# Kernel tuning notes

Hardware: AMD Instinct MI355X
Metric: run time of the kernel (lower is better)

The kernel has to match this reference:

```python
import jax, jax.numpy as jnp
import numpy as np

DT = 0.01
NJ = 7
GRAV = 9.81
Q_LOWER = jnp.array([-2.9671, -1.8326, -2.9671, -3.1416, -2.9671, -0.0873, -2.9671], jnp.float32)
Q_UPPER = jnp.array([ 2.9671,  1.8326,  2.9671,  0.0,     2.9671,  3.8223,  2.9671], jnp.float32)


def _skew(v):
    z = jnp.zeros((), v.dtype)
    return jnp.stack([jnp.stack([z, -v[2], v[1]]),
                      jnp.stack([v[2], z, -v[0]]),
                      jnp.stack([-v[1], v[0], z])])


def _mot_X(E, r):
    # 6x6 spatial motion transform [[E,0],[-E*skew(r),E]]
    zero = jnp.zeros_like(E)
    top = jnp.concatenate([E, zero], axis=1)
    bot = jnp.concatenate([-E @ _skew(r), E], axis=1)
    return jnp.concatenate([top, bot], axis=0)


def _crm(v):
    # spatial motion cross-product matrix for v=[w;v0]
    Sw, Sv = _skew(v[:3]), _skew(v[3:])
    zero = jnp.zeros_like(Sw)
    top = jnp.concatenate([Sw, zero], axis=1)
    bot = jnp.concatenate([Sv, Sw], axis=1)
    return jnp.concatenate([top, bot], axis=0)


def _step_single(x, u, axes, R_tree, p_tree, I_sp):
    dt_ = x.dtype
    q = jnp.clip(x[:NJ], Q_LOWER.astype(dt_), Q_UPPER.astype(dt_))
    qd = x[NJ:]
    # forward kinematics: per-joint 6x6 child<-parent transforms and motion subspaces
    Xups, Ss = [], []
    eye3 = jnp.eye(3, dtype=dt_)
    for i in range(NJ):
        a = axes[i]
        c, s = jnp.cos(q[i]), jnp.sin(q[i])
        R = c * eye3 + s * _skew(a) + (1.0 - c) * jnp.outer(a, a)  # rodrigues
        Xj = _mot_X(R.T, jnp.zeros(3, dt_))
        Xt = _mot_X(R_tree[i], p_tree[i])
        Xups.append(Xj @ Xt)
        Ss.append(jnp.concatenate([a, jnp.zeros(3, dt_)]))
    # RNEA bias force h (qdd=0, gravity, zero base velocity, identity base pose)
    v_prev = jnp.zeros(6, dt_)
    a_prev = jnp.array([0.0, 0.0, 0.0, 0.0, 0.0, GRAV], dt_)  # a_base = -g trick
    fs = []
    for i in range(NJ):
        vJ = Ss[i] * qd[i]
        v = Xups[i] @ v_prev + vJ
        acc = Xups[i] @ a_prev + _crm(v) @ vJ
        Iv = I_sp[i] @ v
        f = I_sp[i] @ acc - _crm(v).T @ Iv  # crf(v) = -crm(v)^T
        fs.append(f)
        v_prev, a_prev = v, acc
    h = [None] * NJ
    for i in range(NJ - 1, -1, -1):
        h[i] = Ss[i] @ fs[i]
        if i > 0:
            fs[i - 1] = fs[i - 1] + Xups[i].T @ fs[i]
    h = jnp.stack(h)
    # CRBA mass matrix (serial chain, parent(i)=i-1)
    Ic = [I_sp[i] for i in range(NJ)]
    M = jnp.zeros((NJ, NJ), dt_)
    for i in range(NJ - 1, -1, -1):
        if i > 0:
            Ic[i - 1] = Ic[i - 1] + Xups[i].T @ Ic[i] @ Xups[i]
        F = Ic[i] @ Ss[i]
        M = M.at[i, i].set(Ss[i] @ F)
        for j in range(i - 1, -1, -1):
            F = Xups[j + 1].T @ F
            mij = Ss[j] @ F
            M = M.at[i, j].set(mij).at[j, i].set(mij)
    M = M + 1e-8 * jnp.eye(NJ, dtype=dt_)
    qdd = jnp.linalg.solve(M, (u - h)[:, None])[:, 0]
    qd_new = qd + DT * qdd
    q_new = q + DT * qd_new
    return jnp.concatenate([q_new, qd_new])


def setup_inputs() -> dict:
    B = 65536
    key = jax.random.key(0)
    k1, k2 = jax.random.split(key)
    x = jax.random.normal(k1, (B, 14), jnp.float32)
    u = jax.random.normal(k2, (B, 7), jnp.float32)
    rng = np.random.default_rng(0)
    # unit joint axes
    axes = rng.normal(size=(NJ, 3))
    axes = axes / np.linalg.norm(axes, axis=1, keepdims=True)
    # orthonormal fixed parent->child rotations (det +1)
    R_tree = np.empty((NJ, 3, 3))
    for i in range(NJ):
        Q, _ = np.linalg.qr(rng.normal(size=(3, 3)))
        if np.linalg.det(Q) < 0:
            Q[:, 0] = -Q[:, 0]
        R_tree[i] = Q
    p_tree = 0.2 * rng.normal(size=(NJ, 3))
    # SPD 6x6 spatial inertias: [[Ibar, m*Cx],[m*Cx^T, m*I3]]
    I_sp = np.empty((NJ, 6, 6))
    for i in range(NJ):
        m = float(rng.uniform(1.0, 5.0))
        c = 0.05 * rng.normal(size=3)
        Cx = np.array([[0, -c[2], c[1]], [c[2], 0, -c[0]], [-c[1], c[0], 0]])
        A = 0.1 * rng.normal(size=(3, 3))
        Ic_ = A @ A.T + 0.05 * np.eye(3)
        Ibar = Ic_ + m * Cx @ Cx.T
        I_sp[i] = np.block([[Ibar, m * Cx], [m * Cx.T, m * np.eye(3)]])
    return {
        "x": x, "u": u,
        "axes": jnp.asarray(axes, jnp.float32),
        "R_tree": jnp.asarray(R_tree, jnp.float32),
        "p_tree": jnp.asarray(p_tree, jnp.float32),
        "I_sp": jnp.asarray(I_sp, jnp.float32),
    }


def reference(x, u, axes, R_tree, p_tree, I_sp):
    return jax.vmap(_step_single, in_axes=(0, 0, None, None, None, None))(
        x, u, axes, R_tree, p_tree, I_sp)
```

## Files before the change

kernel.cpp:

```cpp
#include <hip/hip_runtime.h>
#include <math.h>

#define NJ 7
#define DTF 0.01f
#define GRAVF 9.81f
#define MIX(i,j) ((i)*((i)+1)/2 + (j))
#define SNC  15
#define QST  9

__device__ __forceinline__ void cross3(const float* a, const float* b, float* o){
    o[0] = a[1]*b[2] - a[2]*b[1];
    o[1] = a[2]*b[0] - a[0]*b[2];
    o[2] = a[0]*b[1] - a[1]*b[0];
}
__device__ __forceinline__ void mv3(const float* E, const float* x, float* y){
    y[0] = E[0]*x[0] + E[1]*x[1] + E[2]*x[2];
    y[1] = E[3]*x[0] + E[4]*x[1] + E[5]*x[2];
    y[2] = E[6]*x[0] + E[7]*x[1] + E[8]*x[2];
}
__device__ __forceinline__ void mtv3(const float* E, const float* x, float* y){
    y[0] = E[0]*x[0] + E[3]*x[1] + E[6]*x[2];
    y[1] = E[1]*x[0] + E[4]*x[1] + E[7]*x[2];
    y[2] = E[2]*x[0] + E[5]*x[1] + E[8]*x[2];
}
__device__ __forceinline__ void symv(const float* S, const float* x, float* y){
    y[0] = S[0]*x[0] + S[1]*x[1] + S[2]*x[2];
    y[1] = S[1]*x[0] + S[3]*x[1] + S[4]*x[2];
    y[2] = S[2]*x[0] + S[4]*x[1] + S[5]*x[2];
}
__device__ __forceinline__ void mm3(const float* A, const float* B, float* o){
#pragma unroll
    for (int r = 0; r < 3; r++)
#pragma unroll
        for (int c = 0; c < 3; c++)
            o[r*3+c] = A[r*3]*B[c] + A[r*3+1]*B[3+c] + A[r*3+2]*B[6+c];
}
__device__ __forceinline__ void congr(const float* E, const float* X, float* o){
    float t[9];
#pragma unroll
    for (int r = 0; r < 3; r++)
#pragma unroll
        for (int c = 0; c < 3; c++)
            t[r*3+c] = E[r]*X[c] + E[3+r]*X[3+c] + E[6+r]*X[6+c];
    mm3(t, E, o);
}
__device__ __forceinline__ void makeE(const float* a, const float* __restrict__ Rt,
                                      float s, float c, float* E){
    float omc = 1.0f - c;
    float RT[9];
    RT[0] = c + omc*a[0]*a[0];       RT[1] =  s*a[2] + omc*a[0]*a[1]; RT[2] = -s*a[1] + omc*a[0]*a[2];
    RT[3] = -s*a[2] + omc*a[1]*a[0]; RT[4] = c + omc*a[1]*a[1];       RT[5] =  s*a[0] + omc*a[1]*a[2];
    RT[6] =  s*a[1] + omc*a[2]*a[0]; RT[7] = -s*a[0] + omc*a[2]*a[1]; RT[8] = c + omc*a[2]*a[2];
    float Rl[9];
#pragma unroll
    for (int k = 0; k < 9; k++) Rl[k] = Rt[k];
    mm3(RT, Rl, E);
}
__device__ __forceinline__ void bodyI(const float* __restrict__ g_I, int i,
                                      float* SA, float* h, float& m){
    const float* I6 = g_I + i*36;
    SA[0]=I6[0]; SA[1]=I6[1]; SA[2]=I6[2];
    SA[3]=I6[7]; SA[4]=I6[8]; SA[5]=I6[14];
    h[0]=I6[16]; h[1]=I6[5]; h[2]=I6[9];
    m = I6[21];
}

__constant__ float QL_c[NJ] = {-2.9671f,-1.8326f,-2.9671f,-3.1416f,-2.9671f,-0.0873f,-2.9671f};
__constant__ float QU_c[NJ] = { 2.9671f, 1.8326f, 2.9671f, 0.0f,    2.9671f, 3.8223f, 2.9671f};

__global__ __launch_bounds__(128, 2)
void panda_step(const float* __restrict__ x, const float* __restrict__ u,
                const float* __restrict__ g_ax, const float* __restrict__ g_Rt,
                const float* __restrict__ g_pt, const float* __restrict__ g_I,
                float* __restrict__ out, int B)
{
    __shared__ float s_snc[64*SNC];
    __shared__ float s_q  [64*QST];
    __shared__ float s_qd [64*QST];
    __shared__ float s_rhs[64*QST];

    const int role = threadIdx.x >> 6;
    const int lane = threadIdx.x & 63;
    const int e    = blockIdx.x*64 + lane;
    const bool act = (e < B);

    float a_all[3*NJ], p_all[3*NJ];
#pragma unroll
    for (int j = 0; j < 3*NJ; j++){ a_all[j] = g_ax[j]; p_all[j] = g_pt[j]; }
    float SA[6], hc[3], mc;
    bodyI(g_I, 6, SA, hc, mc);

    float q[NJ], qd[NJ], sn[NJ], cs[NJ], uu[NJ];
    if (act && role == 0){
        const float2* x2 = (const float2*)(x + e*14);
        float xl[14];
#pragma unroll
        for (int i = 0; i < 7; i++){ float2 v = x2[i]; xl[2*i] = v.x; xl[2*i+1] = v.y; }
#pragma unroll
        for (int i = 0; i < NJ; i++){
            q[i]  = fminf(fmaxf(xl[i], QL_c[i]), QU_c[i]);
            qd[i] = xl[NJ + i];
            uu[i] = u[e*NJ + i];
            __sincosf(q[i], &sn[i], &cs[i]);
            s_snc[lane*SNC + i]     = sn[i];
            s_snc[lane*SNC + 7 + i] = cs[i];
            s_q [lane*QST + i]      = q[i];
            s_qd[lane*QST + i]      = qd[i];
        }
    }
    __syncthreads();

    float Mx[28];
    if (act){
      if (role == 1){
        float sn1[NJ], cs1[NJ];
#pragma unroll
        for (int i = 0; i < NJ; i++){
            sn1[i] = s_snc[lane*SNC + i];
            cs1[i] = s_snc[lane*SNC + 7 + i];
        }
        float Fb[6*NJ];
#pragma unroll
        for (int i = NJ-1; i >= 0; --i){
            float a[3] = { a_all[3*i], a_all[3*i+1], a_all[3*i+2] };
            float Ft[3]; symv(SA, a, Ft);
            Fb[i*6+0]=Ft[0]; Fb[i*6+1]=Ft[1]; Fb[i*6+2]=Ft[2];
            Fb[i*6+3] = a[1]*hc[2] - a[2]*hc[1];
            Fb[i*6+4] = a[2]*hc[0] - a[0]*hc[2];
            Fb[i*6+5] = a[0]*hc[1] - a[1]*hc[0];
#pragma unroll
            for (int k = i; k < NJ; ++k)
                Mx[MIX(k,i)] = a[0]*Fb[k*6] + a[1]*Fb[k*6+1] + a[2]*Fb[k*6+2];
            if (i > 0){
                float p[3] = { p_all[3*i], p_all[3*i+1], p_all[3*i+2] };
                float E[9]; makeE(a, g_Rt + 9*i, sn1[i], cs1[i], E);
                float SAm[6], hm[3], mm_;
                bodyI(g_I, i-1, SAm, hm, mm_);
                float Af[9] = {SA[0],SA[1],SA[2], SA[1],SA[3],SA[4], SA[2],SA[4],SA[5]};
                float Ap[9]; congr(E, Af, Ap);
                float hr[3]; mtv3(E, hc, hr);
                float hpd = hr[0]*p[0]+hr[1]*p[1]+hr[2]*p[2];
                float ppd = p[0]*p[0]+p[1]*p[1]+p[2]*p[2];
                float dga = 2.0f*hpd + mc*ppd;
                SA[0] = Ap[0] - 2.0f*p[0]*hr[0] - mc*p[0]*p[0] + dga + SAm[0];
                SA[1] = Ap[1] - p[0]*hr[1] - hr[0]*p[1] - mc*p[0]*p[1] + SAm[1];
                SA[2] = Ap[2] - p[0]*hr[2] - hr[0]*p[2] - mc*p[0]*p[2] + SAm[2];
                SA[3] = Ap[4] - 2.0f*p[1]*hr[1] - mc*p[1]*p[1] + dga + SAm[3];
                SA[4] = Ap[5] - p[1]*hr[2] - hr[1]*p[2] - mc*p[1]*p[2] + SAm[4];
                SA[5] = Ap[8] - 2.0f*p[2]*hr[2] - mc*p[2]*p[2] + dga + SAm[5];
                hc[0] = hr[0] + mc*p[0] + hm[0];
                hc[1] = hr[1] + mc*p[1] + hm[1];
                hc[2] = hr[2] + mc*p[2] + hm[2];
                mc += mm_;
#pragma unroll
                for (int k = i; k < NJ; ++k){
                    float ft[3] = {Fb[k*6+0], Fb[k*6+1], Fb[k*6+2]};
                    float fb2[3] = {Fb[k*6+3], Fb[k*6+4], Fb[k*6+5]};
                    float tm[3], tf[3], cp[3];
                    mtv3(E, ft, tm); mtv3(E, fb2, tf);
                    cross3(p, tf, cp);
                    Fb[k*6+0]=tm[0]+cp[0]; Fb[k*6+1]=tm[1]+cp[1]; Fb[k*6+2]=tm[2]+cp[2];
                    Fb[k*6+3]=tf[0];       Fb[k*6+4]=tf[1];       Fb[k*6+5]=tf[2];
                }
            }
        }
#pragma unroll
        for (int i = 0; i < NJ; i++) Mx[MIX(i,i)] += 1e-8f;
#pragma unroll
        for (int k = 0; k < NJ; k++){
            float d = Mx[MIX(k,k)];
#pragma unroll
            for (int j = 0; j < NJ; j++) if (j < k) d -= Mx[MIX(k,j)]*Mx[MIX(k,j)];
            float linv = __builtin_amdgcn_rsqf(d);
            Mx[MIX(k,k)] = linv;
#pragma unroll
            for (int i2 = k+1; i2 < NJ; i2++){
                float s2 = Mx[MIX(i2,k)];
#pragma unroll
                for (int j = 0; j < NJ; j++) if (j < k) s2 -= Mx[MIX(i2,j)]*Mx[MIX(k,j)];
                Mx[MIX(i2,k)] = s2 * linv;
            }
        }
      } else {
        float Fb[6*NJ];
        float w[3]  = {0.f,0.f,0.f}, vl[3] = {0.f,0.f,0.f};
        float aw[3] = {0.f,0.f,0.f}, avv[3] = {0.f,0.f,GRAVF};
#pragma unroll
        for (int i = 0; i < NJ; ++i){
            float a[3] = { a_all[3*i], a_all[3*i+1], a_all[3*i+2] };
            float p[3] = { p_all[3*i], p_all[3*i+1], p_all[3*i+2] };
            float qdi = qd[i];
            float E[9]; makeE(a, g_Rt + 9*i, sn[i], cs[i], E);
            float tw[3]; mv3(E, w, tw);
            float nw[3] = { tw[0]+a[0]*qdi, tw[1]+a[1]*qdi, tw[2]+a[2]*qdi };
            float cwp[3]; cross3(w, p, cwp);
            float t1[3] = { vl[0]+cwp[0], vl[1]+cwp[1], vl[2]+cwp[2] };
            float nvl[3]; mv3(E, t1, nvl);
            float taw[3]; mv3(E, aw, taw);
            float cna[3]; cross3(nw, a, cna);
            float naw[3] = { taw[0]+qdi*cna[0], taw[1]+qdi*cna[1], taw[2]+qdi*cna[2] };
            float cap[3]; cross3(aw, p, cap);
            float t2[3] = { avv[0]+cap[0], avv[1]+cap[1], avv[2]+cap[2] };
            float tav[3]; mv3(E, t2, tav);
            float cva[3]; cross3(nvl, a, cva);
            float nav[3] = { tav[0]+qdi*cva[0], tav[1]+qdi*cva[1], tav[2]+qdi*cva[2] };
            float SAi[6], hi[3], mi; bodyI(g_I, i, SAi, hi, mi);
            float Ivt[3], Iat[3], hxv[3], hxa[3];
            symv(SAi, nw, Ivt);  cross3(hi, nvl, hxv);
            symv(SAi, naw, Iat); cross3(hi, nav, hxa);
#pragma unroll
            for (int k = 0; k < 3; k++){ Ivt[k] += hxv[k]; Iat[k] += hxa[k]; }
            float hxw[3], hxaw[3];
            cross3(hi, nw, hxw); cross3(hi, naw, hxaw);
            float Ivb[3] = { mi*nvl[0]-hxw[0], mi*nvl[1]-hxw[1], mi*nvl[2]-hxw[2] };
            float Iab[3] = { mi*nav[0]-hxaw[0], mi*nav[1]-hxaw[1], mi*nav[2]-hxaw[2] };
            float c1[3], c2[3], c3[3];
            cross3(nw, Ivt, c1); cross3(nvl, Ivb, c2); cross3(nw, Ivb, c3);
            Fb[i*6+0] = Iat[0]+c1[0]+c2[0];
            Fb[i*6+1] = Iat[1]+c1[1]+c2[1];
            Fb[i*6+2] = Iat[2]+c1[2]+c2[2];
            Fb[i*6+3] = Iab[0]+c3[0];
            Fb[i*6+4] = Iab[1]+c3[1];
            Fb[i*6+5] = Iab[2]+c3[2];
#pragma unroll
            for (int k = 0; k < 3; k++){ w[k]=nw[k]; vl[k]=nvl[k]; aw[k]=naw[k]; avv[k]=nav[k]; }
        }
#pragma unroll
        for (int i = NJ-1; i >= 0; --i){
            float a[3] = { a_all[3*i], a_all[3*i+1], a_all[3*i+2] };
            float f0=Fb[i*6+0], f1=Fb[i*6+1], f2=Fb[i*6+2];
            s_rhs[lane*QST + i] = uu[i] - (a[0]*f0 + a[1]*f1 + a[2]*f2);
            if (i > 0){
                float p[3] = { p_all[3*i], p_all[3*i+1], p_all[3*i+2] };
                float E[9]; makeE(a, g_Rt + 9*i, sn[i], cs[i], E);
                float ftop[3] = {f0, f1, f2};
                float fbot[3] = {Fb[i*6+3], Fb[i*6+4], Fb[i*6+5]};
                float tm[3], tf[3], cp[3];
                mtv3(E, ftop, tm); mtv3(E, fbot, tf);
                cross3(p, tf, cp);
                Fb[(i-1)*6+0] += tm[0]+cp[0];
                Fb[(i-1)*6+1] += tm[1]+cp[1];
                Fb[(i-1)*6+2] += tm[2]+cp[2];
                Fb[(i-1)*6+3] += tf[0];
                Fb[(i-1)*6+4] += tf[1];
                Fb[(i-1)*6+5] += tf[2];
            }
        }
      }
    }

    __syncthreads();

    if (act && role == 1){
        float rhs[NJ];
#pragma unroll
        for (int i = 0; i < NJ; i++) rhs[i] = s_rhs[lane*QST + i];
        float y[NJ];
#pragma unroll
        for (int i = 0; i < NJ; i++){
            float s2 = rhs[i];
#pragma unroll
            for (int j = 0; j < NJ; j++) if (j < i) s2 -= Mx[MIX(i,j)]*y[j];
            y[i] = s2 * Mx[MIX(i,i)];
        }
        float z[NJ];
#pragma unroll
        for (int i = NJ-1; i >= 0; i--){
            float s2 = y[i];
#pragma unroll
            for (int j = NJ-1; j >= 0; j--) if (j > i) s2 -= Mx[MIX(j,i)]*z[j];
            z[i] = s2 * Mx[MIX(i,i)];
        }
        float o14[14];
#pragma unroll
        for (int i = 0; i < NJ; i++){
            float qv  = s_q [lane*QST + i];
            float qdv = s_qd[lane*QST + i];
            float qdn = qdv + DTF*z[i];
            o14[i]      = qv + DTF*qdn;
            o14[NJ + i] = qdn;
        }
        float2* o2 = (float2*)(out + e*14);
#pragma unroll
        for (int i = 0; i < 7; i++){ float2 v; v.x = o14[2*i]; v.y = o14[2*i+1]; o2[i] = v; }
    }
}

extern "C" void kernel_launch(void* const* d_in, const int* in_sizes, int n_in,
                              void* d_out, int out_size, void* d_ws, size_t ws_size,
                              hipStream_t stream) {
    const float* x   = (const float*)d_in[0];
    const float* u   = (const float*)d_in[1];
    const float* ax  = (const float*)d_in[2];
    const float* Rt  = (const float*)d_in[3];
    const float* pt  = (const float*)d_in[4];
    const float* Isp = (const float*)d_in[5];
    float* out = (float*)d_out;
    int B = in_sizes[0] / 14;
    int grid = (B + 63) / 64;
    hipLaunchKernelGGL(panda_step, dim3(grid), dim3(128), 0, stream,
                       x, u, ax, Rt, pt, Isp, out, B);
}
```

Before: 83.13 us.

## Roll joint loops and move per-joint state to LDS to cut registers

Replaces the fully unrolled joint loops with rolled loops that prefetch the next joint's axis, offset, rotation and inertia from global memory into registers one step ahead. The per-element force arrays and mass-matrix entries move from registers into padded shared-memory arrays, and the torque vector is staged in shared memory and updated in place. The aim is to lower VGPR pressure and spilling so more waves fit per CU. The cost is extra LDS traffic, loop overhead and less instruction-level parallelism from the loss of full unrolling.

```diff
diff --git a/kernel.cpp b/kernel.cpp
--- a/kernel.cpp
+++ b/kernel.cpp
@@ -5,8 +5,10 @@
 #define DTF 0.01f
 #define GRAVF 9.81f
 #define MIX(i,j) ((i)*((i)+1)/2 + (j))
+#define MPAD 29
+#define FSTR 43
 #define SNC  15
-#define QST  9
+#define MST  23
 
 __device__ __forceinline__ void cross3(const float* a, const float* b, float* o){
     o[0] = a[1]*b[2] - a[2]*b[1];
@@ -44,16 +46,13 @@
             t[r*3+c] = E[r]*X[c] + E[3+r]*X[3+c] + E[6+r]*X[6+c];
     mm3(t, E, o);
 }
-__device__ __forceinline__ void makeE(const float* a, const float* __restrict__ Rt,
-                                      float s, float c, float* E){
+__device__ __forceinline__ void makeE_reg(const float* a, const float* Rl,
+                                          float s, float c, float* E){
     float omc = 1.0f - c;
     float RT[9];
     RT[0] = c + omc*a[0]*a[0];       RT[1] =  s*a[2] + omc*a[0]*a[1]; RT[2] = -s*a[1] + omc*a[0]*a[2];
     RT[3] = -s*a[2] + omc*a[1]*a[0]; RT[4] = c + omc*a[1]*a[1];       RT[5] =  s*a[0] + omc*a[1]*a[2];
     RT[6] =  s*a[1] + omc*a[2]*a[0]; RT[7] = -s*a[0] + omc*a[2]*a[1]; RT[8] = c + omc*a[2]*a[2];
-    float Rl[9];
-#pragma unroll
-    for (int k = 0; k < 9; k++) Rl[k] = Rt[k];
     mm3(RT, Rl, E);
 }
 __device__ __forceinline__ void bodyI(const float* __restrict__ g_I, int i,
@@ -74,38 +73,51 @@
                 const float* __restrict__ g_pt, const float* __restrict__ g_I,
                 float* __restrict__ out, int B)
 {
-    __shared__ float s_snc[64*SNC];
-    __shared__ float s_q  [64*QST];
-    __shared__ float s_qd [64*QST];
-    __shared__ float s_rhs[64*QST];
+    __shared__ float s_M   [64*MPAD];
+    __shared__ float s_F   [2*64*FSTR];
+    __shared__ float s_snc [64*SNC];
+    __shared__ float s_misc[64*MST];
 
     const int role = threadIdx.x >> 6;
     const int lane = threadIdx.x & 63;
     const int e    = blockIdx.x*64 + lane;
     const bool act = (e < B);
 
-    float a_all[3*NJ], p_all[3*NJ];
-#pragma unroll
-    for (int j = 0; j < 3*NJ; j++){ a_all[j] = g_ax[j]; p_all[j] = g_pt[j]; }
+    float aC[3], pC[3], RC[9];
+    float SAx[6], hx[3], mx;
     float SA[6], hc[3], mc;
-    bodyI(g_I, 6, SA, hc, mc);
-
-    float q[NJ], qd[NJ], sn[NJ], cs[NJ], uu[NJ];
-    if (act && role == 0){
-        const float2* x2 = (const float2*)(x + e*14);
-        float xl[14];
-#pragma unroll
-        for (int i = 0; i < 7; i++){ float2 v = x2[i]; xl[2*i] = v.x; xl[2*i+1] = v.y; }
-#pragma unroll
-        for (int i = 0; i < NJ; i++){
-            q[i]  = fminf(fmaxf(xl[i], QL_c[i]), QU_c[i]);
-            qd[i] = xl[NJ + i];
-            uu[i] = u[e*NJ + i];
-            __sincosf(q[i], &sn[i], &cs[i]);
-            s_snc[lane*SNC + i]     = sn[i];
-            s_snc[lane*SNC + 7 + i] = cs[i];
-            s_q [lane*QST + i]      = q[i];
-            s_qd[lane*QST + i]      = qd[i];
+    float snC = 0.f, csC = 0.f, qdC = 0.f;
+
+    if (role == 1){
+        bodyI(g_I, 6, SA, hc, mc);
+        bodyI(g_I, 5, SAx, hx, mx);
+        aC[0]=g_ax[18]; aC[1]=g_ax[19]; aC[2]=g_ax[20];
+        pC[0]=g_pt[18]; pC[1]=g_pt[19]; pC[2]=g_pt[20];
+#pragma unroll
+        for (int k = 0; k < 9; k++) RC[k] = g_Rt[54+k];
+    } else {
+        bodyI(g_I, 0, SAx, hx, mx);
+        aC[0]=g_ax[0]; aC[1]=g_ax[1]; aC[2]=g_ax[2];
+        pC[0]=g_pt[0]; pC[1]=g_pt[1]; pC[2]=g_pt[2];
+#pragma unroll
+        for (int k = 0; k < 9; k++) RC[k] = g_Rt[k];
+        if (act){
+            const float2* x2 = (const float2*)(x + e*14);
+            float xl[14];
+#pragma unroll
+            for (int i = 0; i < 7; i++){ float2 v = x2[i]; xl[2*i] = v.x; xl[2*i+1] = v.y; }
+#pragma unroll
+            for (int i = 0; i < NJ; i++){
+                float qi  = fminf(fmaxf(xl[i], QL_c[i]), QU_c[i]);
+                float qdi = xl[NJ + i];
+                float s, c; __sincosf(qi, &s, &c);
+                s_snc [lane*SNC + i]      = s;
+                s_snc [lane*SNC + 7 + i]  = c;
+                s_misc[lane*MST + i]      = qi;
+                s_misc[lane*MST + 7 + i]  = qdi;
+                s_misc[lane*MST + 14 + i] = u[e*NJ + i];
+                if (i == 0){ snC = s; csC = c; qdC = qdi; }
+            }
         }
     }
     __syncthreads();
@@ -113,57 +125,71 @@
     float Mx[28];
     if (act){
       if (role == 1){
-        float sn1[NJ], cs1[NJ];
-#pragma unroll
-        for (int i = 0; i < NJ; i++){
-            sn1[i] = s_snc[lane*SNC + i];
-            cs1[i] = s_snc[lane*SNC + 7 + i];
-        }
-        float Fb[6*NJ];
-#pragma unroll
+        float* Fb = &s_F[64*FSTR + lane*FSTR];
+        snC = s_snc[lane*SNC + 6];
+        csC = s_snc[lane*SNC + 13];
+#pragma unroll 1
         for (int i = NJ-1; i >= 0; --i){
-            float a[3] = { a_all[3*i], a_all[3*i+1], a_all[3*i+2] };
-            float Ft[3]; symv(SA, a, Ft);
+            float aN[3], pN[3], RN[9], snN, csN, SAxN[6], hxN[3], mxN;
+            if (i > 0){
+                const int b3 = 3*(i-1), b9 = 9*(i-1);
+                aN[0]=g_ax[b3]; aN[1]=g_ax[b3+1]; aN[2]=g_ax[b3+2];
+                pN[0]=g_pt[b3]; pN[1]=g_pt[b3+1]; pN[2]=g_pt[b3+2];
+#pragma unroll
+                for (int k = 0; k < 9; k++) RN[k] = g_Rt[b9+k];
+                snN = s_snc[lane*SNC + (i-1)];
+                csN = s_snc[lane*SNC + 6 + i];
+                bodyI(g_I, (i >= 2) ? (i-2) : 0, SAxN, hxN, mxN);
+            }
+            float Ft[3]; symv(SA, aC, Ft);
             Fb[i*6+0]=Ft[0]; Fb[i*6+1]=Ft[1]; Fb[i*6+2]=Ft[2];
-            Fb[i*6+3] = a[1]*hc[2] - a[2]*hc[1];
-            Fb[i*6+4] = a[2]*hc[0] - a[0]*hc[2];
-            Fb[i*6+5] = a[0]*hc[1] - a[1]*hc[0];
-#pragma unroll
-            for (int k = i; k < NJ; ++k)
-                Mx[MIX(k,i)] = a[0]*Fb[k*6] + a[1]*Fb[k*6+1] + a[2]*Fb[k*6+2];
+            Fb[i*6+3] = aC[1]*hc[2] - aC[2]*hc[1];
+            Fb[i*6+4] = aC[2]*hc[0] - aC[0]*hc[2];
+            Fb[i*6+5] = aC[0]*hc[1] - aC[1]*hc[0];
+#pragma unroll 1
+            for (int k = i; k < NJ; ++k){
+                float f0=Fb[k*6], f1=Fb[k*6+1], f2=Fb[k*6+2];
+                s_M[lane*MPAD + k*(k+1)/2 + i] = aC[0]*f0 + aC[1]*f1 + aC[2]*f2;
+            }
             if (i > 0){
-                float p[3] = { p_all[3*i], p_all[3*i+1], p_all[3*i+2] };
-                float E[9]; makeE(a, g_Rt + 9*i, sn1[i], cs1[i], E);
-                float SAm[6], hm[3], mm_;
-                bodyI(g_I, i-1, SAm, hm, mm_);
+                float E[9]; makeE_reg(aC, RC, snC, csC, E);
                 float Af[9] = {SA[0],SA[1],SA[2], SA[1],SA[3],SA[4], SA[2],SA[4],SA[5]};
                 float Ap[9]; congr(E, Af, Ap);
                 float hr[3]; mtv3(E, hc, hr);
-                float hpd = hr[0]*p[0]+hr[1]*p[1]+hr[2]*p[2];
-                float ppd = p[0]*p[0]+p[1]*p[1]+p[2]*p[2];
+                float hpd = hr[0]*pC[0]+hr[1]*pC[1]+hr[2]*pC[2];
+                float ppd = pC[0]*pC[0]+pC[1]*pC[1]+pC[2]*pC[2];
                 float dga = 2.0f*hpd + mc*ppd;
-                SA[0] = Ap[0] - 2.0f*p[0]*hr[0] - mc*p[0]*p[0] + dga + SAm[0];
-                SA[1] = Ap[1] - p[0]*hr[1] - hr[0]*p[1] - mc*p[0]*p[1] + SAm[1];
-                SA[2] = Ap[2] - p[0]*hr[2] - hr[0]*p[2] - mc*p[0]*p[2] + SAm[2];
-                SA[3] = Ap[4] - 2.0f*p[1]*hr[1] - mc*p[1]*p[1] + dga + SAm[3];
-                SA[4] = Ap[5] - p[1]*hr[2] - hr[1]*p[2] - mc*p[1]*p[2] + SAm[4];
-                SA[5] = Ap[8] - 2.0f*p[2]*hr[2] - mc*p[2]*p[2] + dga + SAm[5];
-                hc[0] = hr[0] + mc*p[0] + hm[0];
-                hc[1] = hr[1] + mc*p[1] + hm[1];
-                hc[2] = hr[2] + mc*p[2] + hm[2];
-                mc += mm_;
-#pragma unroll
+                SA[0] = Ap[0] - 2.0f*pC[0]*hr[0] - mc*pC[0]*pC[0] + dga + SAx[0];
+                SA[1] = Ap[1] - pC[0]*hr[1] - hr[0]*pC[1] - mc*pC[0]*pC[1] + SAx[1];
+                SA[2] = Ap[2] - pC[0]*hr[2] - hr[0]*pC[2] - mc*pC[0]*pC[2] + SAx[2];
+                SA[3] = Ap[4] - 2.0f*pC[1]*hr[1] - mc*pC[1]*pC[1] + dga + SAx[3];
+                SA[4] = Ap[5] - pC[1]*hr[2] - hr[1]*pC[2] - mc*pC[1]*pC[2] + SAx[4];
+                SA[5] = Ap[8] - 2.0f*pC[2]*hr[2] - mc*pC[2]*pC[2] + dga + SAx[5];
+                hc[0] = hr[0] + mc*pC[0] + hx[0];
+                hc[1] = hr[1] + mc*pC[1] + hx[1];
+                hc[2] = hr[2] + mc*pC[2] + hx[2];
+                mc += mx;
+#pragma unroll 1
                 for (int k = i; k < NJ; ++k){
-                    float ft[3] = {Fb[k*6+0], Fb[k*6+1], Fb[k*6+2]};
+                    float ft[3]  = {Fb[k*6+0], Fb[k*6+1], Fb[k*6+2]};
                     float fb2[3] = {Fb[k*6+3], Fb[k*6+4], Fb[k*6+5]};
                     float tm[3], tf[3], cp[3];
                     mtv3(E, ft, tm); mtv3(E, fb2, tf);
-                    cross3(p, tf, cp);
+                    cross3(pC, tf, cp);
                     Fb[k*6+0]=tm[0]+cp[0]; Fb[k*6+1]=tm[1]+cp[1]; Fb[k*6+2]=tm[2]+cp[2];
                     Fb[k*6+3]=tf[0];       Fb[k*6+4]=tf[1];       Fb[k*6+5]=tf[2];
                 }
-            }
-        }
+#pragma unroll
+                for (int k = 0; k < 3; k++){ aC[k]=aN[k]; pC[k]=pN[k]; hx[k]=hxN[k]; }
+#pragma unroll
+                for (int k = 0; k < 9; k++) RC[k]=RN[k];
+#pragma unroll
+                for (int k = 0; k < 6; k++) SAx[k]=SAxN[k];
+                snC=snN; csC=csN; mx=mxN;
+            }
+        }
+#pragma unroll
+        for (int j = 0; j < 28; j++) Mx[j] = s_M[lane*MPAD + j];
 #pragma unroll
         for (int i = 0; i < NJ; i++) Mx[MIX(i,i)] += 1e-8f;
 #pragma unroll
@@ -182,38 +208,46 @@
             }
         }
       } else {
-        float Fb[6*NJ];
+        float* Fb = &s_F[lane*FSTR];
         float w[3]  = {0.f,0.f,0.f}, vl[3] = {0.f,0.f,0.f};
         float aw[3] = {0.f,0.f,0.f}, avv[3] = {0.f,0.f,GRAVF};
-#pragma unroll
+#pragma unroll 1
         for (int i = 0; i < NJ; ++i){
-            float a[3] = { a_all[3*i], a_all[3*i+1], a_all[3*i+2] };
-            float p[3] = { p_all[3*i], p_all[3*i+1], p_all[3*i+2] };
-            float qdi = qd[i];
-            float E[9]; makeE(a, g_Rt + 9*i, sn[i], cs[i], E);
+            float aN[3], pN[3], RN[9], snN, csN, qdN, SAxN[6], hxN[3], mxN;
+            if (i < NJ-1){
+                const int b3 = 3*(i+1), b9 = 9*(i+1);
+                aN[0]=g_ax[b3]; aN[1]=g_ax[b3+1]; aN[2]=g_ax[b3+2];
+                pN[0]=g_pt[b3]; pN[1]=g_pt[b3+1]; pN[2]=g_pt[b3+2];
+#pragma unroll
+                for (int k = 0; k < 9; k++) RN[k] = g_Rt[b9+k];
+                snN = s_snc [lane*SNC + i + 1];
+                csN = s_snc [lane*SNC + 8 + i];
+                qdN = s_misc[lane*MST + 8 + i];
+                bodyI(g_I, i+1, SAxN, hxN, mxN);
+            }
+            float E[9]; makeE_reg(aC, RC, snC, csC, E);
             float tw[3]; mv3(E, w, tw);
-            float nw[3] = { tw[0]+a[0]*qdi, tw[1]+a[1]*qdi, tw[2]+a[2]*qdi };
-            float cwp[3]; cross3(w, p, cwp);
+            float nw[3] = { tw[0]+aC[0]*qdC, tw[1]+aC[1]*qdC, tw[2]+aC[2]*qdC };
+            float cwp[3]; cross3(w, pC, cwp);
             float t1[3] = { vl[0]+cwp[0], vl[1]+cwp[1], vl[2]+cwp[2] };
             float nvl[3]; mv3(E, t1, nvl);
             float taw[3]; mv3(E, aw, taw);
-            float cna[3]; cross3(nw, a, cna);
-            float naw[3] = { taw[0]+qdi*cna[0], taw[1]+qdi*cna[1], taw[2]+qdi*cna[2] };
-            float cap[3]; cross3(aw, p, cap);
+            float cna[3]; cross3(nw, aC, cna);
+            float naw[3] = { taw[0]+qdC*cna[0], taw[1]+qdC*cna[1], taw[2]+qdC*cna[2] };
+            float cap[3]; cross3(aw, pC, cap);
             float t2[3] = { avv[0]+cap[0], avv[1]+cap[1], avv[2]+cap[2] };
             float tav[3]; mv3(E, t2, tav);
-            float cva[3]; cross3(nvl, a, cva);
-            float nav[3] = { tav[0]+qdi*cva[0], tav[1]+qdi*cva[1], tav[2]+qdi*cva[2] };
-            float SAi[6], hi[3], mi; bodyI(g_I, i, SAi, hi, mi);
+            float cva[3]; cross3(nvl, aC, cva);
+            float nav[3] = { tav[0]+qdC*cva[0], tav[1]+qdC*cva[1], tav[2]+qdC*cva[2] };
             float Ivt[3], Iat[3], hxv[3], hxa[3];
-            symv(SAi, nw, Ivt);  cross3(hi, nvl, hxv);
-            symv(SAi, naw, Iat); cross3(hi, nav, hxa);
+            symv(SAx, nw,  Ivt); cross3(hx, nvl, hxv);
+            symv(SAx, naw, Iat); cross3(hx, nav, hxa);
 #pragma unroll
             for (int k = 0; k < 3; k++){ Ivt[k] += hxv[k]; Iat[k] += hxa[k]; }
             float hxw[3], hxaw[3];
-            cross3(hi, nw, hxw); cross3(hi, naw, hxaw);
-            float Ivb[3] = { mi*nvl[0]-hxw[0], mi*nvl[1]-hxw[1], mi*nvl[2]-hxw[2] };
-            float Iab[3] = { mi*nav[0]-hxaw[0], mi*nav[1]-hxaw[1], mi*nav[2]-hxaw[2] };
+            cross3(hx, nw, hxw); cross3(hx, naw, hxaw);
+            float Ivb[3] = { mx*nvl[0]-hxw[0],  mx*nvl[1]-hxw[1],  mx*nvl[2]-hxw[2]  };
+            float Iab[3] = { mx*nav[0]-hxaw[0], mx*nav[1]-hxaw[1], mx*nav[2]-hxaw[2] };
             float c1[3], c2[3], c3[3];
             cross3(nw, Ivt, c1); cross3(nvl, Ivb, c2); cross3(nw, Ivb, c3);
             Fb[i*6+0] = Iat[0]+c1[0]+c2[0];
@@ -224,26 +258,48 @@
             Fb[i*6+5] = Iab[2]+c3[2];
 #pragma unroll
             for (int k = 0; k < 3; k++){ w[k]=nw[k]; vl[k]=nvl[k]; aw[k]=naw[k]; avv[k]=nav[k]; }
-        }
-#pragma unroll
+            if (i < NJ-1){
+#pragma unroll
+                for (int k = 0; k < 3; k++){ aC[k]=aN[k]; pC[k]=pN[k]; hx[k]=hxN[k]; }
+#pragma unroll
+                for (int k = 0; k < 9; k++) RC[k]=RN[k];
+#pragma unroll
+                for (int k = 0; k < 6; k++) SAx[k]=SAxN[k];
+                snC=snN; csC=csN; qdC=qdN; mx=mxN;
+            }
+        }
+#pragma unroll 1
         for (int i = NJ-1; i >= 0; --i){
-            float a[3] = { a_all[3*i], a_all[3*i+1], a_all[3*i+2] };
+            float aN[3], pN[3], RN[9], snN, csN;
+            if (i > 0){
+                const int b3 = 3*(i-1), b9 = 9*(i-1);
+                aN[0]=g_ax[b3]; aN[1]=g_ax[b3+1]; aN[2]=g_ax[b3+2];
+                pN[0]=g_pt[b3]; pN[1]=g_pt[b3+1]; pN[2]=g_pt[b3+2];
+#pragma unroll
+                for (int k = 0; k < 9; k++) RN[k] = g_Rt[b9+k];
+                snN = s_snc[lane*SNC + (i-1)];
+                csN = s_snc[lane*SNC + 6 + i];
+            }
             float f0=Fb[i*6+0], f1=Fb[i*6+1], f2=Fb[i*6+2];
-            s_rhs[lane*QST + i] = uu[i] - (a[0]*f0 + a[1]*f1 + a[2]*f2);
+            s_misc[lane*MST + 14 + i] -= aC[0]*f0 + aC[1]*f1 + aC[2]*f2;
             if (i > 0){
-                float p[3] = { p_all[3*i], p_all[3*i+1], p_all[3*i+2] };
-                float E[9]; makeE(a, g_Rt + 9*i, sn[i], cs[i], E);
+                float E[9]; makeE_reg(aC, RC, snC, csC, E);
                 float ftop[3] = {f0, f1, f2};
                 float fbot[3] = {Fb[i*6+3], Fb[i*6+4], Fb[i*6+5]};
                 float tm[3], tf[3], cp[3];
                 mtv3(E, ftop, tm); mtv3(E, fbot, tf);
-                cross3(p, tf, cp);
+                cross3(pC, tf, cp);
                 Fb[(i-1)*6+0] += tm[0]+cp[0];
                 Fb[(i-1)*6+1] += tm[1]+cp[1];
                 Fb[(i-1)*6+2] += tm[2]+cp[2];
                 Fb[(i-1)*6+3] += tf[0];
                 Fb[(i-1)*6+4] += tf[1];
                 Fb[(i-1)*6+5] += tf[2];
+#pragma unroll
+                for (int k = 0; k < 3; k++){ aC[k]=aN[k]; pC[k]=pN[k]; }
+#pragma unroll
+                for (int k = 0; k < 9; k++) RC[k]=RN[k];
+                snC=snN; csC=csN;
             }
         }
       }
@@ -252,9 +308,13 @@
     __syncthreads();
 
     if (act && role == 1){
-        float rhs[NJ];
-#pragma unroll
-        for (int i = 0; i < NJ; i++) rhs[i] = s_rhs[lane*QST + i];
+        float rhs[NJ], qv[NJ], qdv[NJ];
+#pragma unroll
+        for (int i = 0; i < NJ; i++){
+            qv [i] = s_misc[lane*MST + i];
+            qdv[i] = s_misc[lane*MST + 7 + i];
+            rhs[i] = s_misc[lane*MST + 14 + i];
+        }
         float y[NJ];
 #pragma unroll
         for (int i = 0; i < NJ; i++){
@@ -274,10 +334,8 @@
         float o14[14];
 #pragma unroll
         for (int i = 0; i < NJ; i++){
-            float qv  = s_q [lane*QST + i];
-            float qdv = s_qd[lane*QST + i];
-            float qdn = qdv + DTF*z[i];
-            o14[i]      = qv + DTF*qdn;
+            float qdn = qdv[i] + DTF*z[i];
+            o14[i]      = qv[i] + DTF*qdn;
             o14[NJ + i] = qdn;
         }
         float2* o2 = (float2*)(out + e*14);
```

Measured after the change: 79.70 us. 1.04x faster.
